# Kernel optimization log

Measured on AMD Instinct MI355X. Metric: run time of the kernel, lower is better.

Reference implementation:

```python
import jax, jax.numpy as jnp
import numpy as np

B, H, W = 16, 180, 240  # dim=(180,240), batch inferred from last event in torch code
N = 8_000_000


def setup_inputs() -> dict:
    key = jax.random.key(0)
    k0, k1, k2, k3, k4 = jax.random.split(key, 5)
    x = jax.random.randint(k0, (N,), 0, W).astype(jnp.float32)
    y = jax.random.randint(k1, (N,), 0, H).astype(jnp.float32)
    t = jax.random.uniform(k2, (N,), dtype=jnp.float32)
    p = (jax.random.randint(k3, (N,), 0, 2) * 2 - 1).astype(jnp.float32)  # polarity in {-1,1}
    # b sorted so events[-1,-1] == B-1, matching how torch code infers B
    b = jnp.sort(jax.random.randint(k4, (N,), 0, B)).astype(jnp.float32)
    events = jnp.stack([x, y, t, p, b], axis=1)  # [N,5]
    return {"events": events}


def reference(events):
    x, y, t, p, b = (events[:, i] for i in range(5))
    bi = b.astype(jnp.int32)

    # per-batch time normalization: t /= max(t within batch)
    tmax = jax.ops.segment_max(t, bi, num_segments=B)
    t = t / tmax[bi]
    p = (p + 1.0) / 2.0  # computed (as in torch) but unused downstream

    # full-res event-count histogram: idx = x + W*y + W*H*b
    idx_c = (x + W * y + W * H * b).astype(jnp.int32)
    container = jnp.zeros(B * H * W, jnp.int32).at[idx_c].add(1, mode="drop")
    container = container.reshape(B, H, W)

    # half-res counter/timer; replicate torch float floordiv exactly:
    # idx = x//2 + (W*y)//4 + (W*H*b)//4
    idx_k = (jnp.floor_divide(x, 2.0)
             + jnp.floor_divide(W * y, 4.0)
             + jnp.floor_divide(W * H * b, 4.0)).astype(jnp.int32)
    nvox = B * (H // 2) * (W // 2)
    counter = jnp.zeros(nvox, jnp.int32).at[idx_k].add(1, mode="drop").astype(jnp.float32)
    timer = jnp.zeros(nvox, jnp.float32).at[idx_k].add(t, mode="drop")
    timer = timer / jnp.where(counter == 0, 1.0, counter)  # mean timestamp per voxel
    counter = counter.reshape(B, H // 2, W // 2)
    timer = timer.reshape(B, H // 2, W // 2)

    # strided diffs on the full-res histogram
    dy = container[:, ::2] - container[:, 1::2]          # [B, H/2, W]
    diff_y = dy[:, :, ::2] + dy[:, :, 1::2]              # [B, H/2, W/2]
    dx = container[:, :, ::2] - container[:, :, 1::2]    # [B, H, W/2]
    diff_x = dx[:, 1::2] + dx[:, ::2]                    # [B, H/2, W/2]

    return container, counter, timer, diff_x, diff_y
```

## Files before the change

### kernel.cpp

```cpp
#include <hip/hip_runtime.h>
#include <stdint.h>

constexpr int NB    = 16;
constexpr int NH    = 180;
constexpr int NW    = 240;
constexpr int FULL  = NB * NH * NW;
constexpr int SEG   = (NH / 2) * (NW / 2);
constexpr int HALF  = NB * SEG;
constexpr int CELLS = NH * NW;
constexpr int H4W   = CELLS / 8;
constexpr int EVT   = 1024;
constexpr int NBPB  = 16;
constexpr int NBLK  = NB * NBPB;
constexpr int RT    = 43;
constexpr int TSX   = SEG + 60;

constexpr int O_TMAX  = 0;
constexpr int O_BLEED = 16;
constexpr int ZFAST   = O_BLEED + HALF;
constexpr int O_BND   = ZFAST;
constexpr int O_PRIV  = O_BND + 32;
constexpr int O_CONT  = O_PRIV;
constexpr int O_TSUMF = O_CONT + FULL;
constexpr int O_CNTFB = O_TSUMF + HALF;
constexpr int ZFALL   = O_CNTFB + HALF;

__global__ __launch_bounds__(256) void k_init(unsigned int* __restrict__ ws, int bound,
                                              const float* __restrict__ ev, int n) {
    int tid = threadIdx.x;
    int i = blockIdx.x * 256 + tid;
    int stride = gridDim.x * 256;
    for (; i < bound; i += stride) ws[i] = 0u;
    if (blockIdx.x == 0 && tid <= NB) {
        int lo = 0, hi = n;
        while (lo < hi) {
            int mid = (lo + hi) >> 1;
            float v = ev[(size_t)5 * mid + 4];
            if (v < (float)tid) lo = mid + 1; else hi = mid;
        }
        ((int*)(ws + O_BND))[tid] = lo;
    }
}

__global__ __launch_bounds__(EVT) void k_merged(const float* __restrict__ ev,
                                                unsigned int* __restrict__ ws,
                                                unsigned int* __restrict__ h4p,
                                                float* __restrict__ tsp) {
    unsigned int* tmaxb   = ws + O_TMAX;
    float*        bleed_g = (float*)(ws + O_BLEED);
    const int*    bnd     = (const int*)(ws + O_BND);

    __shared__ unsigned int h4[H4W];
    __shared__ float        ts[TSX];
    __shared__ unsigned int bsm;
    int tid = threadIdx.x;
    {
        uint4 z = {0u, 0u, 0u, 0u};
        uint4* h4v = (uint4*)h4;
        uint4* tsv = (uint4*)ts;
        for (int i = tid; i < H4W / 4; i += EVT) h4v[i] = z;
        for (int i = tid; i < SEG / 4; i += EVT) tsv[i] = z;
        if (tid < TSX - SEG) ts[SEG + tid] = 0.0f;
        if (tid == 0) bsm = 0u;
    }

    int b0 = blockIdx.x / NBPB;
    int r  = blockIdx.x - b0 * NBPB;
    int sb = bnd[b0], eb = bnd[b0 + 1];
    long long len = (long long)(eb - sb);
    int s = sb + (int)(len * r / NBPB);
    int e = sb + (int)(len * (r + 1) / NBPB);
    __syncthreads();

    float tloc = 0.0f;

    auto proc = [&](float fx, float fy, float t) {
        int xi = (int)fx, yi = (int)fy;
        int cell = xi + NW * yi;
        int loc  = (xi >> 1) + (NW / 4) * yi;
        tloc = fmaxf(tloc, t);
        atomicAdd(&h4[cell >> 3], 1u << ((cell & 7) * 4));
        atomicAdd(&ts[loc], t);
    };

    if (s < e) {
        int as_ = min((s + 3) & ~3, e);
        for (int i = s + tid; i < as_; i += EVT) {
            const float* rr = ev + (size_t)5 * i;
            proc(rr[0], rr[1], rr[2]);
        }
        int ng = (e - as_) >> 2;
        const float4* e4 = (const float4*)ev;
        size_t qbase = (size_t)5 * (size_t)(as_ >> 2);
        for (int g = tid; g < ng; g += 2 * EVT) {
            int g2 = g + EVT;
            size_t qb = qbase + (size_t)5 * g;
            float4 q0 = e4[qb], q1 = e4[qb + 1], q2 = e4[qb + 2],
                   q3 = e4[qb + 3], q4 = e4[qb + 4];
            if (g2 < ng) {
                size_t qc = qbase + (size_t)5 * g2;
                float4 p0 = e4[qc], p1 = e4[qc + 1], p2 = e4[qc + 2],
                       p3 = e4[qc + 3], p4 = e4[qc + 4];
                proc(q0.x, q0.y, q0.z);
                proc(q1.y, q1.z, q1.w);
                proc(q2.z, q2.w, q3.x);
                proc(q3.w, q4.x, q4.y);
                proc(p0.x, p0.y, p0.z);
                proc(p1.y, p1.z, p1.w);
                proc(p2.z, p2.w, p3.x);
                proc(p3.w, p4.x, p4.y);
            } else {
                proc(q0.x, q0.y, q0.z);
                proc(q1.y, q1.z, q1.w);
                proc(q2.z, q2.w, q3.x);
                proc(q3.w, q4.x, q4.y);
            }
        }
        for (int i = as_ + (ng << 2) + tid; i < e; i += EVT) {
            const float* rr = ev + (size_t)5 * i;
            proc(rr[0], rr[1], rr[2]);
        }
    }

#pragma unroll
    for (int o = 32; o > 0; o >>= 1) tloc = fmaxf(tloc, __shfl_xor(tloc, o));
    if ((tid & 63) == 0) atomicMax(&bsm, __float_as_uint(tloc));
    __syncthreads();

    {
        const uint4* h4v = (const uint4*)h4;
        const uint4* tsv = (const uint4*)ts;
        uint4* dh = (uint4*)(h4p + (size_t)blockIdx.x * H4W);
        uint4* dt = (uint4*)(tsp + (size_t)blockIdx.x * SEG);
        for (int i = tid; i < H4W / 4; i += EVT) dh[i] = h4v[i];
        for (int i = tid; i < SEG / 4; i += EVT) dt[i] = tsv[i];
    }
    if (b0 < NB - 1 && tid < 60) {
        float v = ts[SEG + tid];
        if (v != 0.0f) atomicAdd(&bleed_g[(b0 + 1) * SEG + tid], v);
    }
    if (tid == 0 && bsm) atomicMax(&tmaxb[b0], bsm);
}

__global__ __launch_bounds__(256) void k_reduce(const unsigned int* __restrict__ ws,
                                                const unsigned int* __restrict__ h4p,
                                                const float* __restrict__ tsp,
                                                float* __restrict__ out) {
    const unsigned int* tmaxb   = ws + O_TMAX;
    const float*        bleed_g = (const float*)(ws + O_BLEED);

    int tid  = threadIdx.x;
    int b    = blockIdx.x / RT;
    int tile = blockIdx.x - b * RT;

    int rem = tile * 256 + tid;
    if (rem >= SEG) return;
    int v = b * SEG + rem;
    int i = rem / (NW / 2);
    int j = rem - i * (NW / 2);
    int cbl = 480 * i + 2 * j;
    int cbg = CELLS * b + cbl;

    unsigned c00 = 0, c01 = 0, c10 = 0, c11 = 0, oc = 0;
    float tsum = 0.0f;

    bool prev = false;
    int ocell;
    if (j >= 60)      ocell = cbl + 120;
    else if (i >= 1)  ocell = cbl - 120;
    else { prev = true; ocell = 43080 + 2 * j; }

    int w0i = cbl >> 3, nib = (cbl & 7) * 4;
    int w1i = w0i + 30;
    int owi = ocell >> 3, onib = (ocell & 7) * 4;

    int base = b * NBPB;
#pragma unroll
    for (int k = 0; k < NBPB; ++k) {
        const unsigned int* hp = h4p + (size_t)(base + k) * H4W;
        unsigned w0 = hp[w0i], w1 = hp[w1i], wo = hp[owi];
        float tv = tsp[(size_t)(base + k) * SEG + rem];
        c00 += (w0 >> nib) & 15u;  c01 += (w0 >> (nib + 4)) & 15u;
        c10 += (w1 >> nib) & 15u;  c11 += (w1 >> (nib + 4)) & 15u;
        oc  += ((wo >> onib) & 15u) + ((wo >> (onib + 4)) & 15u);
        tsum += tv;
    }
    if (prev) {
        oc = 0;
        if (b >= 1) {
            int pb = (b - 1) * NBPB;
#pragma unroll
            for (int k = 0; k < NBPB; ++k) {
                unsigned wo = h4p[(size_t)(pb + k) * H4W + owi];
                oc += ((wo >> onib) & 15u) + ((wo >> (onib + 4)) & 15u);
            }
        }
    }
    unsigned cnt = c00 + c01 + oc;

    out[cbg]          = (float)c00;
    out[cbg + 1]      = (float)c01;
    out[cbg + NW]     = (float)c10;
    out[cbg + NW + 1] = (float)c11;
    out[FULL + v] = (float)cnt;

    float tm = __uint_as_float(tmaxb[b]);
    if (!(tm > 0.0f)) tm = 1.0f;
    float tmp = (b > 0) ? __uint_as_float(tmaxb[b - 1]) : 1.0f;
    if (!(tmp > 0.0f)) tmp = 1.0f;
    float s = tsum / tm + bleed_g[v] / tmp;
    out[FULL + HALF + v] = s / (float)(cnt == 0 ? 1u : cnt);

    out[FULL + 2 * HALF + v] = (float)((int)c00 - (int)c01 + (int)c10 - (int)c11);
    out[FULL + 3 * HALF + v] = (float)((int)c00 + (int)c01 - (int)c10 - (int)c11);
}


__global__ __launch_bounds__(256) void f_events(const float* __restrict__ ev, int n,
                                                unsigned int* __restrict__ ws) {
    unsigned int* tmaxb = ws + O_TMAX;
    int*   cont  = (int*)(ws + O_CONT);
    int*   cnt   = (int*)(ws + O_CNTFB);
    float* tsum  = (float*)(ws + O_TSUMF);
    float* bleed = (float*)(ws + O_BLEED);
    __shared__ unsigned int smax[NB];
    if (threadIdx.x < NB) smax[threadIdx.x] = 0u;
    __syncthreads();
    int chunk = (n + gridDim.x - 1) / (int)gridDim.x;
    int start = blockIdx.x * chunk;
    int end   = min(start + chunk, n);
    for (int i = start + (int)threadIdx.x; i < end; i += (int)blockDim.x) {
        const float* r = ev + (size_t)5 * (size_t)i;
        int xi = (int)r[0], yi = (int)r[1], bi = (int)r[4];
        float t = r[2];
        atomicMax(&smax[bi], __float_as_uint(t));
        atomicAdd(&cont[xi + NW * yi + CELLS * bi], 1);
        int loc = (xi >> 1) + (NW / 4) * yi;
        int ik  = loc + SEG * bi;
        if (ik < HALF) {
            atomicAdd(&cnt[ik], 1);
            if (loc >= SEG) atomicAdd(&bleed[ik], t);
            else            atomicAdd(&tsum[ik], t);
        }
    }
    __syncthreads();
    if (threadIdx.x < NB) {
        unsigned v = smax[threadIdx.x];
        if (v) atomicMax(&tmaxb[threadIdx.x], v);
    }
}

__global__ __launch_bounds__(256) void f_epilogue(const unsigned int* __restrict__ ws,
                                                  float* __restrict__ out) {
    const unsigned int* tmaxb = ws + O_TMAX;
    const int*   cont  = (const int*)(ws + O_CONT);
    const int*   cnt   = (const int*)(ws + O_CNTFB);
    const float* tsum  = (const float*)(ws + O_TSUMF);
    const float* bleed = (const float*)(ws + O_BLEED);
    int v = blockIdx.x * blockDim.x + threadIdx.x;
    if (v >= HALF) return;
    int b   = v / SEG;
    int rem = v - b * SEG;
    int i   = rem / (NW / 2);
    int j   = rem - i * (NW / 2);
    int cbase = b * CELLS + 480 * i + 2 * j;
    int c00 = cont[cbase],      c01 = cont[cbase + 1];
    int c10 = cont[cbase + NW], c11 = cont[cbase + NW + 1];
    out[cbase]          = (float)c00;
    out[cbase + 1]      = (float)c01;
    out[cbase + NW]     = (float)c10;
    out[cbase + NW + 1] = (float)c11;
    int c = cnt[v];
    out[FULL + v] = (float)c;
    float tm  = __uint_as_float(tmaxb[b]);
    if (!(tm > 0.0f)) tm = 1.0f;
    float tmp = (b > 0) ? __uint_as_float(tmaxb[b - 1]) : 1.0f;
    if (!(tmp > 0.0f)) tmp = 1.0f;
    float s   = tsum[v] / tm + bleed[v] / tmp;
    out[FULL + HALF + v] = s / (float)(c == 0 ? 1 : c);
    out[FULL + 2 * HALF + v] = (float)(c00 - c01 + c10 - c11);
    out[FULL + 3 * HALF + v] = (float)(c00 + c01 - c10 - c11);
}

extern "C" void kernel_launch(void* const* d_in, const int* in_sizes, int n_in,
                              void* d_out, int out_size, void* d_ws, size_t ws_size,
                              hipStream_t stream) {
    const float* ev = (const float*)d_in[0];
    int n = in_sizes[0] / 5;
    unsigned int* ws = (unsigned int*)d_ws;
    float* out = (float*)d_out;

    size_t need = (size_t)(O_PRIV + NBLK * (H4W + SEG)) * 4u;

    if (ws_size >= need && n > 0) {
        unsigned int* h4p = ws + O_PRIV;
        float*        tsp = (float*)(ws + O_PRIV + NBLK * H4W);
        hipLaunchKernelGGL(k_init, dim3(64), dim3(256), 0, stream, ws, ZFAST, ev, n);
        hipLaunchKernelGGL(k_merged, dim3(NBLK), dim3(EVT), 0, stream, ev, ws, h4p, tsp);
        hipLaunchKernelGGL(k_reduce, dim3(NB * RT), dim3(256), 0, stream, ws, h4p, tsp, out);
    } else {
        hipLaunchKernelGGL(k_init, dim3(512), dim3(256), 0, stream, ws, ZFALL, ev, n);
        hipLaunchKernelGGL(f_events, dim3(2048), dim3(256), 0, stream, ev, n, ws);
        hipLaunchKernelGGL(f_epilogue, dim3((HALF + 255) / 256), dim3(256), 0, stream, ws, out);
    }
}
```

Before: 249.1 us.

## Drop init kernel by computing bounds per block and storing per-block tmax/bleed

Removes the separate zero-init and boundary-search kernel in the fast path. Each merged block now binary-searches its own batch bounds while the remaining threads zero shared memory. Instead of global atomics into zeroed buffers, each block writes its tmax and 60 bleed values to per-block slots, and the reduce kernel combines them. This saves a kernel launch and the zeroing pass, at the cost of a redundant binary search in every block and a few extra loads in the reduce.

```diff
diff --git a/kernel.cpp b/kernel.cpp
--- a/kernel.cpp
+++ b/kernel.cpp
@@ -15,62 +15,56 @@
 constexpr int RT    = 43;
 constexpr int TSX   = SEG + 60;
 
-constexpr int O_TMAX  = 0;
-constexpr int O_BLEED = 16;
-constexpr int ZFAST   = O_BLEED + HALF;
-constexpr int O_BND   = ZFAST;
-constexpr int O_PRIV  = O_BND + 32;
-constexpr int O_CONT  = O_PRIV;
-constexpr int O_TSUMF = O_CONT + FULL;
-constexpr int O_CNTFB = O_TSUMF + HALF;
-constexpr int ZFALL   = O_CNTFB + HALF;
-
-__global__ __launch_bounds__(256) void k_init(unsigned int* __restrict__ ws, int bound,
-                                              const float* __restrict__ ev, int n) {
+constexpr int O_TMAXB = 0;
+constexpr int O_BLDP  = NBLK;
+constexpr int O_PRIV  = O_BLDP + NBLK * 60;
+constexpr int FB_TMAX  = 0;
+constexpr int FB_BLEED = 16;
+constexpr int FB_CONT  = FB_BLEED + HALF;
+constexpr int FB_TSUM  = FB_CONT + FULL;
+constexpr int FB_CNT   = FB_TSUM + HALF;
+constexpr int ZFALL    = FB_CNT + HALF;
+
+__global__ __launch_bounds__(EVT) void k_merged(const float* __restrict__ ev, int n,
+                                                unsigned int* __restrict__ ws,
+                                                unsigned int* __restrict__ h4p,
+                                                float* __restrict__ tsp) {
+    float* tmax_blk = (float*)(ws + O_TMAXB);
+    float* bleed_p  = (float*)(ws + O_BLDP);
+
+    __shared__ unsigned int h4[H4W];
+    __shared__ float        ts[TSX];
+    __shared__ int          sbe[2];
+    __shared__ unsigned int bsm;
     int tid = threadIdx.x;
-    int i = blockIdx.x * 256 + tid;
-    int stride = gridDim.x * 256;
-    for (; i < bound; i += stride) ws[i] = 0u;
-    if (blockIdx.x == 0 && tid <= NB) {
+    int b0 = blockIdx.x / NBPB;
+    int r  = blockIdx.x - b0 * NBPB;
+
+    if (tid < 2) {
+        int target = b0 + tid;
         int lo = 0, hi = n;
         while (lo < hi) {
             int mid = (lo + hi) >> 1;
             float v = ev[(size_t)5 * mid + 4];
-            if (v < (float)tid) lo = mid + 1; else hi = mid;
-        }
-        ((int*)(ws + O_BND))[tid] = lo;
-    }
-}
-
-__global__ __launch_bounds__(EVT) void k_merged(const float* __restrict__ ev,
-                                                unsigned int* __restrict__ ws,
-                                                unsigned int* __restrict__ h4p,
-                                                float* __restrict__ tsp) {
-    unsigned int* tmaxb   = ws + O_TMAX;
-    float*        bleed_g = (float*)(ws + O_BLEED);
-    const int*    bnd     = (const int*)(ws + O_BND);
-
-    __shared__ unsigned int h4[H4W];
-    __shared__ float        ts[TSX];
-    __shared__ unsigned int bsm;
-    int tid = threadIdx.x;
-    {
+            if (v < (float)target) lo = mid + 1; else hi = mid;
+        }
+        sbe[tid] = lo;
+    } else {
         uint4 z = {0u, 0u, 0u, 0u};
         uint4* h4v = (uint4*)h4;
         uint4* tsv = (uint4*)ts;
-        for (int i = tid; i < H4W / 4; i += EVT) h4v[i] = z;
-        for (int i = tid; i < SEG / 4; i += EVT) tsv[i] = z;
-        if (tid < TSX - SEG) ts[SEG + tid] = 0.0f;
-        if (tid == 0) bsm = 0u;
-    }
-
-    int b0 = blockIdx.x / NBPB;
-    int r  = blockIdx.x - b0 * NBPB;
-    int sb = bnd[b0], eb = bnd[b0 + 1];
+        int t2 = tid - 2;
+        for (int i = t2; i < H4W / 4; i += EVT - 2) h4v[i] = z;
+        for (int i = t2; i < SEG / 4; i += EVT - 2) tsv[i] = z;
+        if (t2 < TSX - SEG) ts[SEG + t2] = 0.0f;
+        if (tid == 2) bsm = 0u;
+    }
+    __syncthreads();
+
+    int sb = sbe[0], eb = sbe[1];
     long long len = (long long)(eb - sb);
     int s = sb + (int)(len * r / NBPB);
     int e = sb + (int)(len * (r + 1) / NBPB);
-    __syncthreads();
 
     float tloc = 0.0f;
 
@@ -135,23 +129,32 @@
         for (int i = tid; i < H4W / 4; i += EVT) dh[i] = h4v[i];
         for (int i = tid; i < SEG / 4; i += EVT) dt[i] = tsv[i];
     }
-    if (b0 < NB - 1 && tid < 60) {
-        float v = ts[SEG + tid];
-        if (v != 0.0f) atomicAdd(&bleed_g[(b0 + 1) * SEG + tid], v);
-    }
-    if (tid == 0 && bsm) atomicMax(&tmaxb[b0], bsm);
+    if (tid < 60) bleed_p[blockIdx.x * 60 + tid] = ts[SEG + tid];
+    if (tid == 0) tmax_blk[blockIdx.x] = __uint_as_float(bsm);
 }
 
 __global__ __launch_bounds__(256) void k_reduce(const unsigned int* __restrict__ ws,
                                                 const unsigned int* __restrict__ h4p,
                                                 const float* __restrict__ tsp,
                                                 float* __restrict__ out) {
-    const unsigned int* tmaxb   = ws + O_TMAX;
-    const float*        bleed_g = (const float*)(ws + O_BLEED);
-
+    const float* tmax_blk = (const float*)(ws + O_TMAXB);
+    const float* bleed_p  = (const float*)(ws + O_BLDP);
+
+    __shared__ float stm[2];
     int tid  = threadIdx.x;
     int b    = blockIdx.x / RT;
     int tile = blockIdx.x - b * RT;
+
+    if (tid < 32) {
+        int which = tid >> 4;
+        int k = tid & 15;
+        int bb = b - which;
+        float v = (bb >= 0) ? tmax_blk[bb * NBPB + k] : 0.0f;
+#pragma unroll
+        for (int o = 8; o > 0; o >>= 1) v = fmaxf(v, __shfl_xor(v, o));
+        if (k == 0) stm[which] = v;
+    }
+    __syncthreads();
 
     int rem = tile * 256 + tid;
     if (rem >= SEG) return;
@@ -162,7 +165,7 @@
     int cbg = CELLS * b + cbl;
 
     unsigned c00 = 0, c01 = 0, c10 = 0, c11 = 0, oc = 0;
-    float tsum = 0.0f;
+    float tsum = 0.0f, bl = 0.0f;
 
     bool prev = false;
     int ocell;
@@ -193,6 +196,7 @@
             for (int k = 0; k < NBPB; ++k) {
                 unsigned wo = h4p[(size_t)(pb + k) * H4W + owi];
                 oc += ((wo >> onib) & 15u) + ((wo >> (onib + 4)) & 15u);
+                bl += bleed_p[(pb + k) * 60 + j];
             }
         }
     }
@@ -204,11 +208,11 @@
     out[cbg + NW + 1] = (float)c11;
     out[FULL + v] = (float)cnt;
 
-    float tm = __uint_as_float(tmaxb[b]);
+    float tm = stm[0];
     if (!(tm > 0.0f)) tm = 1.0f;
-    float tmp = (b > 0) ? __uint_as_float(tmaxb[b - 1]) : 1.0f;
+    float tmp = stm[1];
     if (!(tmp > 0.0f)) tmp = 1.0f;
-    float s = tsum / tm + bleed_g[v] / tmp;
+    float s = tsum / tm + bl / tmp;
     out[FULL + HALF + v] = s / (float)(cnt == 0 ? 1u : cnt);
 
     out[FULL + 2 * HALF + v] = (float)((int)c00 - (int)c01 + (int)c10 - (int)c11);
@@ -216,13 +220,19 @@
 }
 
 
+__global__ __launch_bounds__(256) void f_init(unsigned int* __restrict__ ws, int bound) {
+    int i = blockIdx.x * 256 + threadIdx.x;
+    int stride = gridDim.x * 256;
+    for (; i < bound; i += stride) ws[i] = 0u;
+}
+
 __global__ __launch_bounds__(256) void f_events(const float* __restrict__ ev, int n,
                                                 unsigned int* __restrict__ ws) {
-    unsigned int* tmaxb = ws + O_TMAX;
-    int*   cont  = (int*)(ws + O_CONT);
-    int*   cnt   = (int*)(ws + O_CNTFB);
-    float* tsum  = (float*)(ws + O_TSUMF);
-    float* bleed = (float*)(ws + O_BLEED);
+    unsigned int* tmaxb = ws + FB_TMAX;
+    int*   cont  = (int*)(ws + FB_CONT);
+    int*   cnt   = (int*)(ws + FB_CNT);
+    float* tsum  = (float*)(ws + FB_TSUM);
+    float* bleed = (float*)(ws + FB_BLEED);
     __shared__ unsigned int smax[NB];
     if (threadIdx.x < NB) smax[threadIdx.x] = 0u;
     __syncthreads();
@@ -252,11 +262,11 @@
 
 __global__ __launch_bounds__(256) void f_epilogue(const unsigned int* __restrict__ ws,
                                                   float* __restrict__ out) {
-    const unsigned int* tmaxb = ws + O_TMAX;
-    const int*   cont  = (const int*)(ws + O_CONT);
-    const int*   cnt   = (const int*)(ws + O_CNTFB);
-    const float* tsum  = (const float*)(ws + O_TSUMF);
-    const float* bleed = (const float*)(ws + O_BLEED);
+    const unsigned int* tmaxb = ws + FB_TMAX;
+    const int*   cont  = (const int*)(ws + FB_CONT);
+    const int*   cnt   = (const int*)(ws + FB_CNT);
+    const float* tsum  = (const float*)(ws + FB_TSUM);
+    const float* bleed = (const float*)(ws + FB_BLEED);
     int v = blockIdx.x * blockDim.x + threadIdx.x;
     if (v >= HALF) return;
     int b   = v / SEG;
@@ -295,11 +305,10 @@
     if (ws_size >= need && n > 0) {
         unsigned int* h4p = ws + O_PRIV;
         float*        tsp = (float*)(ws + O_PRIV + NBLK * H4W);
-        hipLaunchKernelGGL(k_init, dim3(64), dim3(256), 0, stream, ws, ZFAST, ev, n);
-        hipLaunchKernelGGL(k_merged, dim3(NBLK), dim3(EVT), 0, stream, ev, ws, h4p, tsp);
+        hipLaunchKernelGGL(k_merged, dim3(NBLK), dim3(EVT), 0, stream, ev, n, ws, h4p, tsp);
         hipLaunchKernelGGL(k_reduce, dim3(NB * RT), dim3(256), 0, stream, ws, h4p, tsp, out);
     } else {
-        hipLaunchKernelGGL(k_init, dim3(512), dim3(256), 0, stream, ws, ZFALL, ev, n);
+        hipLaunchKernelGGL(f_init, dim3(512), dim3(256), 0, stream, ws, ZFALL);
         hipLaunchKernelGGL(f_events, dim3(2048), dim3(256), 0, stream, ev, n, ws);
         hipLaunchKernelGGL(f_epilogue, dim3((HALF + 255) / 256), dim3(256), 0, stream, ws, out);
     }
```

New measurement: 244.5 us. No clear change (-1.8%).
